# Performance work log

Measured on AMD Instinct MI355X. Metric: run time of the kernel, lower is better.

Reference implementation:

```python
import jax, jax.numpy as jnp
import numpy as np

B, IDF, RES = 32, 64, 128
CDF, SRC_L, A_DIM = 768, 18, 100
QUERY_L = RES * RES


def setup_inputs() -> dict:
    key = jax.random.key(0)
    ks = jax.random.split(key, 5)
    inputs = jax.random.normal(ks[0], (B, IDF, RES, RES), dtype=jnp.float32)
    context = jax.random.normal(ks[1], (B, CDF, SRC_L), dtype=jnp.float32)
    conv_ctx_w = jax.random.normal(ks[2], (IDF, CDF), dtype=jnp.float32) * (1.0 / np.sqrt(CDF))
    conv_w = jax.random.normal(ks[3], (IDF,), dtype=jnp.float32) * (1.0 / np.sqrt(IDF))
    conv_b = jnp.zeros((1,), dtype=jnp.float32)
    fc_w = jax.random.normal(ks[4], (A_DIM, QUERY_L), dtype=jnp.float32) * (1.0 / np.sqrt(QUERY_L))
    fc_b = jnp.zeros((A_DIM,), dtype=jnp.float32)
    return {"inputs": inputs, "context": context, "conv_ctx_w": conv_ctx_w,
            "conv_w": conv_w, "conv_b": conv_b, "fc_w": fc_w, "fc_b": fc_b}


def reference(inputs, context, conv_ctx_w, conv_w, conv_b, fc_w, fc_b):
    b, idf, ih, iw = inputs.shape
    queryL = ih * iw
    # target: [b, idf, queryL]
    target = inputs.reshape(b, idf, queryL)
    # 1x1 conv on context (conv_context): [b, idf, sourceL]
    sourceT = jnp.einsum('ic,bcs->bis', conv_ctx_w, context)
    # attn scores: [b, queryL, sourceL]; softmax over sourceL (dim=1 on flattened view)
    attn = jnp.einsum('biq,bis->bqs', target, sourceT)
    attn = jax.nn.softmax(attn, axis=-1)
    # weighted context: [b, idf, queryL]
    wctx = jnp.einsum('bis,bqs->biq', sourceT, attn)
    # 1x1 conv to single channel (self.conv): [b, queryL]
    wctx = jnp.einsum('i,biq->bq', conv_w, wctx) + conv_b
    # att_fc: [b, a_dim]
    out = wctx @ fc_w.T + fc_b
    return out
```

## Files before the change

### kernel.cpp

```cpp
#include <hip/hip_runtime.h>

#define BB 32
#define IDF 64
#define QL 16384
#define CDF 768
#define SL 18
#define SLP 20
#define ADIM 100

__global__ __launch_bounds__(256, 2) void kA_source(
        const float* __restrict__ ctx,
        const float* __restrict__ wic,
        const float* __restrict__ fc_b,
        float* __restrict__ sT,
        float* __restrict__ out)
{
    const int blk  = blockIdx.x;
    const int tid  = threadIdx.x;
    const int wave = tid >> 6;
    const int lane = tid & 63;

    if (blk < 13) {
        const int t = blk * 256 + tid;
        if (t < BB * ADIM) out[t] = fc_b[t % ADIM];
    }

    const int b = blk >> 4;
    const int i = (blk & 15) * 4 + wave;
    const float* ctxb = ctx + (size_t)b * CDF * SL;
    const float* wrow = wic + (size_t)i * CDF;

    float acc[SL];
#pragma unroll
    for (int s = 0; s < SL; s++) acc[s] = 0.f;

#pragma unroll 2
    for (int k = 0; k < CDF / 64; k++) {
        const int c = k * 64 + lane;
        const float wv = wrow[c];
        const float* cr = ctxb + (size_t)c * SL;
        float r[SL];
#pragma unroll
        for (int s = 0; s < SL; s++) r[s] = cr[s];
#pragma unroll
        for (int s = 0; s < SL; s++) acc[s] += wv * r[s];
    }
#pragma unroll
    for (int s = 0; s < SL; s++) {
        float a = acc[s];
#pragma unroll
        for (int off = 32; off; off >>= 1) a += __shfl_xor(a, off, 64);
        if (lane == 0) sT[((size_t)b * IDF + i) * SLP + s] = a;
    }
}

__global__ __launch_bounds__(256, 2) void kB_attn_fc(
        const float* __restrict__ inp,
        const float* __restrict__ sT,
        const float* __restrict__ conv_w,
        const float* __restrict__ conv_b,
        const float* __restrict__ fcw,
        float* __restrict__ out)
{
    __shared__ __align__(16) float st_l[IDF * SLP];
    __shared__ __align__(16) float wq_l[512];
    __shared__ float cw_l[IDF];
    __shared__ float v_l[SL];
    const int b   = blockIdx.y;
    const int qt  = blockIdx.x;
    const int tid = threadIdx.x;
    const int wave = tid >> 6;
    const int lane = tid & 63;

    for (int t = tid; t < IDF * SLP; t += 256) st_l[t] = sT[(size_t)b * IDF * SLP + t];
    if (tid < IDF) cw_l[tid] = conv_w[tid];
    __syncthreads();
    if (tid < SL) {
        float a = 0.f;
#pragma unroll
        for (int i = 0; i < IDF; i++) a += cw_l[i] * st_l[i * SLP + tid];
        v_l[tid] = a;
    }
    __syncthreads();

    const float2* ip2 = (const float2*)(inp + (size_t)b * IDF * QL + (size_t)qt * 512);

    float2 sc[SL];
#pragma unroll
    for (int s = 0; s < SL; s++) sc[s] = make_float2(0.f, 0.f);

    float2 xb[4];
#pragma unroll
    for (int j = 0; j < 4; j++) xb[j] = ip2[(size_t)j * (QL / 2) + tid];

#pragma unroll 4
    for (int i = 0; i < IDF; i++) {
        const float2 x = xb[i & 3];
        if (i + 4 < IDF) xb[i & 3] = ip2[(size_t)(i + 4) * (QL / 2) + tid];
        float r[SL];
        const float4* r4 = (const float4*)&st_l[i * SLP];
        ((float4*)r)[0] = r4[0];
        ((float4*)r)[1] = r4[1];
        ((float4*)r)[2] = r4[2];
        ((float4*)r)[3] = r4[3];
        ((float2*)(r + 16))[0] = *(const float2*)&st_l[i * SLP + 16];
#pragma unroll
        for (int s = 0; s < SL; s++) {
            sc[s].x += x.x * r[s];
            sc[s].y += x.y * r[s];
        }
    }

    float2 m = sc[0];
#pragma unroll
    for (int s = 1; s < SL; s++) {
        m.x = fmaxf(m.x, sc[s].x);
        m.y = fmaxf(m.y, sc[s].y);
    }
    float2 l = make_float2(0.f, 0.f);
    float2 o = make_float2(0.f, 0.f);
#pragma unroll
    for (int s = 0; s < SL; s++) {
        const float vs = v_l[s];
        float2 p;
        p.x = __expf(sc[s].x - m.x);
        p.y = __expf(sc[s].y - m.y);
        l.x += p.x; l.y += p.y;
        o.x += p.x * vs; o.y += p.y * vs;
    }
    const float cb = conv_b[0];
    float2 res;
    res.x = o.x / l.x + cb;
    res.y = o.y / l.y + cb;
    ((float2*)wq_l)[tid] = res;
    __syncthreads();

    float wv[8];
    ((float4*)wv)[0] = *(const float4*)&wq_l[lane * 8];
    ((float4*)wv)[1] = *(const float4*)&wq_l[lane * 8 + 4];

    const float* fcw_t = fcw + (size_t)qt * 512;
#pragma unroll 1
    for (int aa = 0; aa < 25; aa++) {
        const int a = wave * 25 + aa;
        const float* fr = fcw_t + (size_t)a * QL + lane * 8;
        float4 f0 = *(const float4*)fr;
        float4 f1 = *(const float4*)(fr + 4);
        float acc = f0.x * wv[0] + f0.y * wv[1] + f0.z * wv[2] + f0.w * wv[3]
                  + f1.x * wv[4] + f1.y * wv[5] + f1.z * wv[6] + f1.w * wv[7];
#pragma unroll
        for (int off = 32; off; off >>= 1) acc += __shfl_xor(acc, off, 64);
        if (lane == 0) atomicAdd(&out[b * ADIM + a], acc);
    }
}

extern "C" void kernel_launch(void* const* d_in, const int* in_sizes, int n_in,
                              void* d_out, int out_size, void* d_ws, size_t ws_size,
                              hipStream_t stream)
{
    const float* inputs     = (const float*)d_in[0];
    const float* context    = (const float*)d_in[1];
    const float* conv_ctx_w = (const float*)d_in[2];
    const float* conv_w     = (const float*)d_in[3];
    const float* conv_b     = (const float*)d_in[4];
    const float* fc_w       = (const float*)d_in[5];
    const float* fc_b       = (const float*)d_in[6];
    float* out = (float*)d_out;

    float* ws = (float*)d_ws;
    float* sT = ws;

    kA_source<<<dim3(512), dim3(256), 0, stream>>>(context, conv_ctx_w, fc_b, sT, out);
    kB_attn_fc<<<dim3(32, BB), dim3(256), 0, stream>>>(inputs, sT, conv_w, conv_b, fc_w, out);
}
```

Baseline: 239.7 us.

## Group four batches per block to reuse fc_w rows and stage context in LDS

The attention+FC kernel now gives each 512-thread block four batches, one query per thread. It loops over the batches serially and reuses each loaded fc_w slice for all four batch dot products. This cuts fc_w traffic fourfold compared with one batch per block. The source kernel now stages the per-batch context into padded shared memory before the projection. In exchange, the grid drops to 256 large blocks, which lowers occupancy and latency hiding, and the batch loop is serial.

```diff
diff --git a/kernel.cpp b/kernel.cpp
--- a/kernel.cpp
+++ b/kernel.cpp
@@ -6,6 +6,7 @@
 #define CDF 768
 #define SL 18
 #define SLP 20
+#define CLP 21
 #define ADIM 100
 
 __global__ __launch_bounds__(256, 2) void kA_source(
@@ -15,19 +16,28 @@
         float* __restrict__ sT,
         float* __restrict__ out)
 {
+    __shared__ float ctx_l[CDF * CLP];
     const int blk  = blockIdx.x;
     const int tid  = threadIdx.x;
     const int wave = tid >> 6;
     const int lane = tid & 63;
+    const int b = blk >> 4;
+    const int g = blk & 15;
 
     if (blk < 13) {
         const int t = blk * 256 + tid;
         if (t < BB * ADIM) out[t] = fc_b[t % ADIM];
     }
 
-    const int b = blk >> 4;
-    const int i = (blk & 15) * 4 + wave;
     const float* ctxb = ctx + (size_t)b * CDF * SL;
+    for (int t = tid; t < CDF * SL; t += 256) {
+        const int c = t / SL;
+        const int s = t - c * SL;
+        ctx_l[c * CLP + s] = ctxb[t];
+    }
+    __syncthreads();
+
+    const int i = g * 4 + wave;
     const float* wrow = wic + (size_t)i * CDF;
 
     float acc[SL];
@@ -38,12 +48,8 @@
     for (int k = 0; k < CDF / 64; k++) {
         const int c = k * 64 + lane;
         const float wv = wrow[c];
-        const float* cr = ctxb + (size_t)c * SL;
-        float r[SL];
 #pragma unroll
-        for (int s = 0; s < SL; s++) r[s] = cr[s];
-#pragma unroll
-        for (int s = 0; s < SL; s++) acc[s] += wv * r[s];
+        for (int s = 0; s < SL; s++) acc[s] += wv * ctx_l[c * CLP + s];
     }
 #pragma unroll
     for (int s = 0; s < SL; s++) {
@@ -54,7 +60,7 @@
     }
 }
 
-__global__ __launch_bounds__(256, 2) void kB_attn_fc(
+__global__ __launch_bounds__(512, 2) void kB_attn_fc(
         const float* __restrict__ inp,
         const float* __restrict__ sT,
         const float* __restrict__ conv_w,
@@ -62,95 +68,102 @@
         const float* __restrict__ fcw,
         float* __restrict__ out)
 {
-    __shared__ __align__(16) float st_l[IDF * SLP];
-    __shared__ __align__(16) float wq_l[512];
+    __shared__ __align__(16) float st_l[4][IDF * SLP];
+    __shared__ __align__(16) float wq_l[4][512];
     __shared__ float cw_l[IDF];
-    __shared__ float v_l[SL];
-    const int b   = blockIdx.y;
+    __shared__ float v_l[4][SL];
     const int qt  = blockIdx.x;
+    const int bg  = blockIdx.y;
     const int tid = threadIdx.x;
     const int wave = tid >> 6;
     const int lane = tid & 63;
 
-    for (int t = tid; t < IDF * SLP; t += 256) st_l[t] = sT[(size_t)b * IDF * SLP + t];
+    for (int t = tid; t < 4 * IDF * SLP; t += 512) {
+        const int bb = t / (IDF * SLP);
+        const int r  = t - bb * (IDF * SLP);
+        st_l[bb][r] = sT[((size_t)(bg * 4 + bb) * IDF * SLP) + r];
+    }
     if (tid < IDF) cw_l[tid] = conv_w[tid];
     __syncthreads();
-    if (tid < SL) {
+    if (tid < 4 * SL) {
+        const int bb = tid / SL;
+        const int s  = tid - bb * SL;
         float a = 0.f;
 #pragma unroll
-        for (int i = 0; i < IDF; i++) a += cw_l[i] * st_l[i * SLP + tid];
-        v_l[tid] = a;
+        for (int i = 0; i < IDF; i++) a += cw_l[i] * st_l[bb][i * SLP + s];
+        v_l[bb][s] = a;
     }
     __syncthreads();
 
-    const float2* ip2 = (const float2*)(inp + (size_t)b * IDF * QL + (size_t)qt * 512);
+    const int q = qt * 512 + tid;
+    const float cb = conv_b[0];
 
-    float2 sc[SL];
+#pragma unroll 1
+    for (int bb = 0; bb < 4; bb++) {
+        const float* ip = inp + ((size_t)(bg * 4 + bb) * IDF) * QL + q;
+
+        float xa[8];
 #pragma unroll
-    for (int s = 0; s < SL; s++) sc[s] = make_float2(0.f, 0.f);
+        for (int j = 0; j < 8; j++) xa[j] = ip[(size_t)j * QL];
 
-    float2 xb[4];
+        float sc[SL];
 #pragma unroll
-    for (int j = 0; j < 4; j++) xb[j] = ip2[(size_t)j * (QL / 2) + tid];
+        for (int s = 0; s < SL; s++) sc[s] = 0.f;
 
-#pragma unroll 4
-    for (int i = 0; i < IDF; i++) {
-        const float2 x = xb[i & 3];
-        if (i + 4 < IDF) xb[i & 3] = ip2[(size_t)(i + 4) * (QL / 2) + tid];
-        float r[SL];
-        const float4* r4 = (const float4*)&st_l[i * SLP];
-        ((float4*)r)[0] = r4[0];
-        ((float4*)r)[1] = r4[1];
-        ((float4*)r)[2] = r4[2];
-        ((float4*)r)[3] = r4[3];
-        ((float2*)(r + 16))[0] = *(const float2*)&st_l[i * SLP + 16];
+#pragma unroll 8
+        for (int i = 0; i < IDF; i++) {
+            const float x = xa[i & 7];
+            if (i + 8 < IDF) xa[i & 7] = ip[(size_t)(i + 8) * QL];
+            float r[SLP];
+            const float4* r4 = (const float4*)&st_l[bb][i * SLP];
+            ((float4*)r)[0] = r4[0];
+            ((float4*)r)[1] = r4[1];
+            ((float4*)r)[2] = r4[2];
+            ((float4*)r)[3] = r4[3];
+            ((float2*)(r + 16))[0] = *(const float2*)&st_l[bb][i * SLP + 16];
+#pragma unroll
+            for (int s = 0; s < SL; s++) sc[s] += x * r[s];
+        }
+
+        float m = sc[0];
+#pragma unroll
+        for (int s = 1; s < SL; s++) m = fmaxf(m, sc[s]);
+        float l = 0.f, o = 0.f;
 #pragma unroll
         for (int s = 0; s < SL; s++) {
-            sc[s].x += x.x * r[s];
-            sc[s].y += x.y * r[s];
+            const float p = __expf(sc[s] - m);
+            l += p;
+            o += p * v_l[bb][s];
         }
+        wq_l[bb][tid] = o / l + cb;
+    }
+    __syncthreads();
+
+    float wv[4][8];
+#pragma unroll
+    for (int bb = 0; bb < 4; bb++) {
+        ((float4*)wv[bb])[0] = *(const float4*)&wq_l[bb][lane * 8];
+        ((float4*)wv[bb])[1] = *(const float4*)&wq_l[bb][lane * 8 + 4];
     }
 
-    float2 m = sc[0];
+    const float* fcw_t = fcw + (size_t)qt * 512 + lane * 8;
+#pragma unroll 1
+    for (int a = wave; a < ADIM; a += 8) {
+        const float* fr = fcw_t + (size_t)a * QL;
+        const float4 f0 = *(const float4*)fr;
+        const float4 f1 = *(const float4*)(fr + 4);
+        float f[8];
+        ((float4*)f)[0] = f0;
+        ((float4*)f)[1] = f1;
 #pragma unroll
-    for (int s = 1; s < SL; s++) {
-        m.x = fmaxf(m.x, sc[s].x);
-        m.y = fmaxf(m.y, sc[s].y);
-    }
-    float2 l = make_float2(0.f, 0.f);
-    float2 o = make_float2(0.f, 0.f);
+        for (int bb = 0; bb < 4; bb++) {
+            float acc = 0.f;
 #pragma unroll
-    for (int s = 0; s < SL; s++) {
-        const float vs = v_l[s];
-        float2 p;
-        p.x = __expf(sc[s].x - m.x);
-        p.y = __expf(sc[s].y - m.y);
-        l.x += p.x; l.y += p.y;
-        o.x += p.x * vs; o.y += p.y * vs;
-    }
-    const float cb = conv_b[0];
-    float2 res;
-    res.x = o.x / l.x + cb;
-    res.y = o.y / l.y + cb;
-    ((float2*)wq_l)[tid] = res;
-    __syncthreads();
-
-    float wv[8];
-    ((float4*)wv)[0] = *(const float4*)&wq_l[lane * 8];
-    ((float4*)wv)[1] = *(const float4*)&wq_l[lane * 8 + 4];
-
-    const float* fcw_t = fcw + (size_t)qt * 512;
-#pragma unroll 1
-    for (int aa = 0; aa < 25; aa++) {
-        const int a = wave * 25 + aa;
-        const float* fr = fcw_t + (size_t)a * QL + lane * 8;
-        float4 f0 = *(const float4*)fr;
-        float4 f1 = *(const float4*)(fr + 4);
-        float acc = f0.x * wv[0] + f0.y * wv[1] + f0.z * wv[2] + f0.w * wv[3]
-                  + f1.x * wv[4] + f1.y * wv[5] + f1.z * wv[6] + f1.w * wv[7];
+            for (int j = 0; j < 8; j++) acc += f[j] * wv[bb][j];
 #pragma unroll
-        for (int off = 32; off; off >>= 1) acc += __shfl_xor(acc, off, 64);
-        if (lane == 0) atomicAdd(&out[b * ADIM + a], acc);
+            for (int off = 32; off; off >>= 1) acc += __shfl_xor(acc, off, 64);
+            if (lane == 0) atomicAdd(&out[(bg * 4 + bb) * ADIM + a], acc);
+        }
     }
 }
 
@@ -171,5 +184,5 @@
     float* sT = ws;
 
     kA_source<<<dim3(512), dim3(256), 0, stream>>>(context, conv_ctx_w, fc_b, sT, out);
-    kB_attn_fc<<<dim3(32, BB), dim3(256), 0, stream>>>(inputs, sT, conv_w, conv_b, fc_w, out);
+    kB_attn_fc<<<dim3(32, 8), dim3(512), 0, stream>>>(inputs, sT, conv_w, conv_b, fc_w, out);
 }
```

Measured after the change: 324.4 us. 35.3% more time.

## Split FC into separate batched kernel and stage context in LDS

Applied to the files above, without the earlier changes.

The fused attention+FC kernel is split in two. The attention kernel now writes per-query weighted values to a workspace, and a new kC_fc kernel computes the FC as a small GEMM that reuses each fc_w load across 8 batches. Before, every batch block re-read fc_w, which is about 6.5MB per batch. kA_source also stages the context tile in padded shared memory instead of doing strided global loads per lane. The cost is an extra kernel launch and a 2MB workspace round trip.

```diff
diff --git a/kernel.cpp b/kernel.cpp
--- a/kernel.cpp
+++ b/kernel.cpp
@@ -6,6 +6,7 @@
 #define CDF 768
 #define SL 18
 #define SLP 20
+#define CLP 21
 #define ADIM 100
 
 __global__ __launch_bounds__(256, 2) void kA_source(
@@ -15,19 +16,28 @@
         float* __restrict__ sT,
         float* __restrict__ out)
 {
+    __shared__ float ctx_l[CDF * CLP];
     const int blk  = blockIdx.x;
     const int tid  = threadIdx.x;
     const int wave = tid >> 6;
     const int lane = tid & 63;
+    const int b = blk >> 4;
+    const int g = blk & 15;
 
     if (blk < 13) {
         const int t = blk * 256 + tid;
         if (t < BB * ADIM) out[t] = fc_b[t % ADIM];
     }
 
-    const int b = blk >> 4;
-    const int i = (blk & 15) * 4 + wave;
     const float* ctxb = ctx + (size_t)b * CDF * SL;
+    for (int t = tid; t < CDF * SL; t += 256) {
+        const int c = t / SL;
+        const int s = t - c * SL;
+        ctx_l[c * CLP + s] = ctxb[t];
+    }
+    __syncthreads();
+
+    const int i = g * 4 + wave;
     const float* wrow = wic + (size_t)i * CDF;
 
     float acc[SL];
@@ -38,12 +48,8 @@
     for (int k = 0; k < CDF / 64; k++) {
         const int c = k * 64 + lane;
         const float wv = wrow[c];
-        const float* cr = ctxb + (size_t)c * SL;
-        float r[SL];
-#pragma unroll
-        for (int s = 0; s < SL; s++) r[s] = cr[s];
-#pragma unroll
-        for (int s = 0; s < SL; s++) acc[s] += wv * r[s];
+#pragma unroll
+        for (int s = 0; s < SL; s++) acc[s] += wv * ctx_l[c * CLP + s];
     }
 #pragma unroll
     for (int s = 0; s < SL; s++) {
@@ -54,23 +60,19 @@
     }
 }
 
-__global__ __launch_bounds__(256, 2) void kB_attn_fc(
+__global__ __launch_bounds__(256, 2) void kB_attn(
         const float* __restrict__ inp,
         const float* __restrict__ sT,
         const float* __restrict__ conv_w,
         const float* __restrict__ conv_b,
-        const float* __restrict__ fcw,
-        float* __restrict__ out)
+        float* __restrict__ wq)
 {
     __shared__ __align__(16) float st_l[IDF * SLP];
-    __shared__ __align__(16) float wq_l[512];
     __shared__ float cw_l[IDF];
     __shared__ float v_l[SL];
     const int b   = blockIdx.y;
     const int qt  = blockIdx.x;
     const int tid = threadIdx.x;
-    const int wave = tid >> 6;
-    const int lane = tid & 63;
 
     for (int t = tid; t < IDF * SLP; t += 256) st_l[t] = sT[(size_t)b * IDF * SLP + t];
     if (tid < IDF) cw_l[tid] = conv_w[tid];
@@ -132,25 +134,57 @@
     float2 res;
     res.x = o.x / l.x + cb;
     res.y = o.y / l.y + cb;
-    ((float2*)wq_l)[tid] = res;
-    __syncthreads();
-
-    float wv[8];
-    ((float4*)wv)[0] = *(const float4*)&wq_l[lane * 8];
-    ((float4*)wv)[1] = *(const float4*)&wq_l[lane * 8 + 4];
-
-    const float* fcw_t = fcw + (size_t)qt * 512;
-#pragma unroll 1
-    for (int aa = 0; aa < 25; aa++) {
-        const int a = wave * 25 + aa;
-        const float* fr = fcw_t + (size_t)a * QL + lane * 8;
-        float4 f0 = *(const float4*)fr;
-        float4 f1 = *(const float4*)(fr + 4);
-        float acc = f0.x * wv[0] + f0.y * wv[1] + f0.z * wv[2] + f0.w * wv[3]
-                  + f1.x * wv[4] + f1.y * wv[5] + f1.z * wv[6] + f1.w * wv[7];
-#pragma unroll
-        for (int off = 32; off; off >>= 1) acc += __shfl_xor(acc, off, 64);
-        if (lane == 0) atomicAdd(&out[b * ADIM + a], acc);
+    ((float2*)(wq + (size_t)b * QL + (size_t)qt * 512))[tid] = res;
+}
+
+__global__ __launch_bounds__(320, 2) void kC_fc(
+        const float* __restrict__ wq,
+        const float* __restrict__ fcw,
+        float* __restrict__ out)
+{
+    const int blk = blockIdx.x;
+    const int bg  = blk / 80;
+    const int rem = blk - bg * 80;
+    const int ag  = rem >> 3;
+    const int qc  = rem & 7;
+    const int wave = threadIdx.x >> 6;
+    const int lane = threadIdx.x & 63;
+    const int a0 = ag * 10 + wave * 2;
+    const int b0 = bg * 8;
+    const int q0 = qc * 2048;
+
+    float acc[2][8];
+#pragma unroll
+    for (int j = 0; j < 2; j++)
+#pragma unroll
+        for (int i = 0; i < 8; i++) acc[j][i] = 0.f;
+
+#pragma unroll 2
+    for (int k = 0; k < 8; k++) {
+        const int qi = q0 + (k * 64 + lane) * 4;
+        float4 fv[2];
+#pragma unroll
+        for (int j = 0; j < 2; j++) fv[j] = *(const float4*)(fcw + (size_t)(a0 + j) * QL + qi);
+        float4 wv[8];
+#pragma unroll
+        for (int i = 0; i < 8; i++) wv[i] = *(const float4*)(wq + (size_t)(b0 + i) * QL + qi);
+#pragma unroll
+        for (int j = 0; j < 2; j++)
+#pragma unroll
+            for (int i = 0; i < 8; i++)
+                acc[j][i] += fv[j].x * wv[i].x + fv[j].y * wv[i].y
+                           + fv[j].z * wv[i].z + fv[j].w * wv[i].w;
+    }
+
+#pragma unroll
+    for (int j = 0; j < 2; j++) {
+#pragma unroll
+        for (int i = 0; i < 8; i++) {
+            float r = acc[j][i];
+#pragma unroll
+            for (int off = 32; off; off >>= 1) r += __shfl_xor(r, off, 64);
+            if (lane == 0) atomicAdd(&out[(b0 + i) * ADIM + a0 + j], r);
+        }
     }
 }
 
@@ -169,7 +203,9 @@
 
     float* ws = (float*)d_ws;
     float* sT = ws;
+    float* wq = ws + (size_t)BB * IDF * SLP;
 
     kA_source<<<dim3(512), dim3(256), 0, stream>>>(context, conv_ctx_w, fc_b, sT, out);
-    kB_attn_fc<<<dim3(32, BB), dim3(256), 0, stream>>>(inputs, sT, conv_w, conv_b, fc_w, out);
-}
+    kB_attn<<<dim3(32, BB), dim3(256), 0, stream>>>(inputs, sT, conv_w, conv_b, wq);
+    kC_fc<<<dim3(320), dim3(320), 0, stream>>>(wq, fc_w, out);
+}
```

New measurement: 238.3 us. Within noise of the previous version (-0.6%).
